# Kernel tuning notes

Hardware: AMD Instinct MI355X
Metric: run time of the kernel (lower is better)

Reference implementation:

```python
import math
import jax, jax.numpy as jnp
import numpy as np

EMBED_DIM = 1024
NUM_HEADS = 16
FACTOR = 5


def setup_inputs() -> dict:
    key = jax.random.key(0)
    kx, kw, kb, kow, kob = jax.random.split(key, 5)
    B, S, E = 8, 4096, EMBED_DIM
    scale = 1.0 / math.sqrt(E)
    x = jax.random.normal(kx, (B, S, E), dtype=jnp.float32)
    # nn.MultiheadAttention params: packed in_proj (q,k,v) and out_proj
    in_proj_w = jax.random.uniform(kw, (3 * E, E), dtype=jnp.float32, minval=-scale, maxval=scale)
    in_proj_b = jnp.zeros((3 * E,), dtype=jnp.float32)
    out_w = jax.random.uniform(kow, (E, E), dtype=jnp.float32, minval=-scale, maxval=scale)
    out_b = jnp.zeros((E,), dtype=jnp.float32)
    return {"x": x, "in_proj_w": in_proj_w, "in_proj_b": in_proj_b, "out_w": out_w, "out_b": out_b}


def reference(x, in_proj_w, in_proj_b, out_w, out_b):
    B, S, E = x.shape
    H = NUM_HEADS
    hd = E // H
    k = max(1, int(FACTOR * math.log(S + 1)))
    k = min(k, S)

    # top-k queries by L2 norm of each token
    energy = jnp.linalg.norm(x, axis=-1)            # [B, S]
    _, topk_idx = jax.lax.top_k(energy, k)          # [B, k]

    q_tok = jnp.take_along_axis(x, topk_idx[..., None], axis=1)  # [B, k, E]

    Wq, Wk, Wv = jnp.split(in_proj_w, 3, axis=0)    # each [E, E]
    bq, bk, bv = jnp.split(in_proj_b, 3, axis=0)

    q = (q_tok @ Wq.T + bq).reshape(B, k, H, hd)    # [B, k, H, hd]
    kk = (x @ Wk.T + bk).reshape(B, S, H, hd)       # [B, S, H, hd]
    v = (x @ Wv.T + bv).reshape(B, S, H, hd)

    scores = jnp.einsum("bqhd,bshd->bhqs", q, kk) / math.sqrt(hd)
    attn = jax.nn.softmax(scores, axis=-1)          # [B, H, k, S]
    ctx = jnp.einsum("bhqs,bshd->bqhd", attn, v).reshape(B, k, E)
    out_sel = ctx @ out_w.T + out_b                 # [B, k, E]

    # default value for non-selected positions: per-batch mean of x
    default = jnp.mean(x, axis=1)                   # [B, E]
    result = jnp.broadcast_to(default[:, None, :], (B, S, E))
    batch_ar = jnp.arange(B)[:, None]
    result = result.at[batch_ar, topk_idx].set(out_sel)
    return result
```

## Files before the change

kernel.cpp:

```cpp
#include <hip/hip_runtime.h>

using u16 = unsigned short;
using u32 = unsigned int;
using u64 = unsigned long long;
typedef __attribute__((ext_vector_type(8))) short s16x8;
typedef __attribute__((ext_vector_type(4))) short s16x4;
typedef __attribute__((ext_vector_type(4))) float f32x4;

__device__ __forceinline__ float bf2f(u16 u){ return __uint_as_float(((u32)u)<<16); }
__device__ __forceinline__ u16 f2bf(float f){
  u32 u = __float_as_uint(f);
  u += 0x7fffu + ((u>>16)&1u);
  return (u16)(u>>16);
}
__device__ __forceinline__ void gl_lds16(const void* g, void* l){
  __builtin_amdgcn_global_load_lds((const __attribute__((address_space(1))) void*)g,
                                   (__attribute__((address_space(3))) void*)l, 16, 0, 0);
}

__global__ __launch_bounds__(256) void k_cvt_all(const float* __restrict__ ipw, const float* __restrict__ ipb,
                                                 const float* __restrict__ outw,
                                                 u16* __restrict__ ipwb, u16* __restrict__ ipbb,
                                                 u16* __restrict__ outwb){
  int bid = blockIdx.x;
  const float* src; u16* dst; int n; int base;
  if (bid < 3072){ src=ipw; dst=ipwb; n=3145728; base=bid; }
  else if (bid < 3075){ src=ipb; dst=ipbb; n=3072; base=bid-3072; }
  else { src=outw; dst=outwb; n=1048576; base=bid-3075; }
  int i = (base*256 + threadIdx.x)*4;
  if (i >= n) return;
  float4 v = *(const float4*)(src + i);
  s16x4 o;
  o[0]=(short)f2bf(v.x); o[1]=(short)f2bf(v.y); o[2]=(short)f2bf(v.z); o[3]=(short)f2bf(v.w);
  *(s16x4*)(dst + i) = o;
}

__global__ __launch_bounds__(256) void k_prep_x(const float* __restrict__ x, u16* __restrict__ xb, float* __restrict__ energy){
  int tok = blockIdx.x*4 + (threadIdx.x>>6);
  int lane = threadIdx.x & 63;
  const float* p = x + (size_t)tok*1024 + lane*16;
  float4 a[4];
  #pragma unroll
  for (int j=0;j<4;++j) a[j] = ((const float4*)p)[j];
  float s = 0.f;
  s16x8 o0, o1;
  #pragma unroll
  for (int j=0;j<2;++j){
    o0[j*4+0]=(short)f2bf(a[j].x); o0[j*4+1]=(short)f2bf(a[j].y);
    o0[j*4+2]=(short)f2bf(a[j].z); o0[j*4+3]=(short)f2bf(a[j].w);
  }
  #pragma unroll
  for (int j=0;j<2;++j){
    o1[j*4+0]=(short)f2bf(a[2+j].x); o1[j*4+1]=(short)f2bf(a[2+j].y);
    o1[j*4+2]=(short)f2bf(a[2+j].z); o1[j*4+3]=(short)f2bf(a[2+j].w);
  }
  #pragma unroll
  for (int j=0;j<4;++j){
    s += a[j].x*a[j].x + a[j].y*a[j].y + a[j].z*a[j].z + a[j].w*a[j].w;
  }
  u16* xo = xb + (size_t)tok*1024 + lane*16;
  *(s16x8*)xo = o0;
  *(s16x8*)(xo+8) = o1;
  #pragma unroll
  for (int off=32; off; off>>=1) s += __shfl_xor(s, off);
  if (lane==0) energy[tok] = s;
}

__global__ __launch_bounds__(256) void k_colsum(const u16* __restrict__ xb, float* __restrict__ colsum){
  int b = blockIdx.x, sc = blockIdx.y;
  int t = threadIdx.x;
  float acc[4] = {0.f,0.f,0.f,0.f};
  for (int s = sc*128; s < sc*128+128; ++s){
    s16x4 v = *(const s16x4*)(xb + ((size_t)b*4096 + s)*1024 + t*4);
    #pragma unroll
    for (int i=0;i<4;++i) acc[i] += bf2f((u16)v[i]);
  }
  #pragma unroll
  for (int i=0;i<4;++i) atomicAdd(&colsum[b*1024 + t*4 + i], acc[i]);
}

__global__ __launch_bounds__(256) void k_topk(const float* __restrict__ energy, int* __restrict__ topk, int* __restrict__ sel){
  int b = blockIdx.x, t = threadIdx.x;
  int lane = t & 63, wid = t >> 6;
  __shared__ u64 wmax[4];
  __shared__ u64 winner;
  u64 v[16];
  #pragma unroll
  for (int i=0;i<16;++i){
    u32 tok = i*256 + t;
    float e = energy[b*4096 + tok];
    v[i] = ((u64)__float_as_uint(e) << 32) | (u32)(~tok);
    sel[b*4096 + tok] = -1;
  }
  __syncthreads();
  for (int it=0; it<41; ++it){
    u64 m = v[0];
    #pragma unroll
    for (int i=1;i<16;++i) m = v[i] > m ? v[i] : m;
    #pragma unroll
    for (int off=32; off; off>>=1){
      u64 o = __shfl_xor(m, off);
      m = o > m ? o : m;
    }
    if (lane==0) wmax[wid] = m;
    __syncthreads();
    if (t==0){
      u64 g = wmax[0];
      #pragma unroll
      for (int w=1;w<4;++w) g = wmax[w] > g ? wmax[w] : g;
      winner = g;
      u32 tok = (~(u32)g) & 4095u;
      topk[b*64+it] = (int)tok;
      sel[b*4096 + tok] = it;
    }
    __syncthreads();
    u32 wtok = (~(u32)winner) & 4095u;
    #pragma unroll
    for (int i=0;i<16;++i){
      if ((u32)(i*256 + t) == wtok) v[i] = 0;
    }
  }
}

__global__ __launch_bounds__(256) void k_gather_q(const float* __restrict__ x, const int* __restrict__ topk,
                                                  u16* __restrict__ Aq){
  int b = blockIdx.x, qi = blockIdx.y, t = threadIdx.x;
  size_t dst = ((size_t)(b*48+qi))*1024 + t*4;
  if (qi >= 41){ s16x4 z = {0,0,0,0}; *(s16x4*)&Aq[dst] = z; return; }
  int tok = topk[b*64+qi];
  float4 v = *(const float4*)(x + ((size_t)b*4096 + tok)*1024 + t*4);
  s16x4 o;
  o[0]=(short)f2bf(v.x); o[1]=(short)f2bf(v.y); o[2]=(short)f2bf(v.z); o[3]=(short)f2bf(v.w);
  *(s16x4*)&Aq[dst] = o;
}

__global__ __launch_bounds__(256) void k_gemm(const u16* __restrict__ A, const u16* __restrict__ Bk,
                                              const u16* __restrict__ Bv,
                                              const u16* __restrict__ biask, const u16* __restrict__ biasv,
                                              u16* __restrict__ C, int nbn, int ncols, int half, float cscale){
  __shared__ u16 As[128*64];
  __shared__ u16 Bs[128*64];
  const int tid = threadIdx.x;
  const int bn = blockIdx.x % nbn;
  const int bm = blockIdx.x / nbn;
  const int m0 = bm*128, n0 = bn*128;
  const u16* Bbase  = (n0 < half) ? (Bk + (size_t)n0*1024) : (Bv + (size_t)(n0-half)*1024);
  const u16* biasp  = (n0 < half) ? (biask + n0) : (biasv + (n0-half));
  const int lane = tid & 63;
  const int wave = tid >> 6;
  const int wr = wave >> 1, wc = wave & 1;
  const int fr = lane & 15;
  const int fq = lane >> 4;
  f32x4 acc[4][4] = {};
  for (int k0 = 0; k0 < 1024; k0 += 64){
    __syncthreads();
    #pragma unroll
    for (int j=0;j<4;++j){
      int idx = j*256 + tid;
      int r = idx>>3; int cc = (idx&7)*8;
      gl_lds16(A + (size_t)(m0+r)*1024 + k0 + cc, &As[r*64+cc]);
    }
    #pragma unroll
    for (int j=0;j<4;++j){
      int idx = j*256 + tid;
      int r = idx>>3; int cc = (idx&7)*8;
      gl_lds16(Bbase + (size_t)r*1024 + k0 + cc, &Bs[r*64+cc]);
    }
    __syncthreads();
    #pragma unroll
    for (int kk=0; kk<64; kk+=32){
      s16x8 af[4], bfv[4];
      #pragma unroll
      for (int m=0;m<4;++m) af[m] = *(const s16x8*)&As[(wr*64 + m*16 + fr)*64 + kk + fq*8];
      #pragma unroll
      for (int n=0;n<4;++n) bfv[n] = *(const s16x8*)&Bs[(wc*64 + n*16 + fr)*64 + kk + fq*8];
      #pragma unroll
      for (int m=0;m<4;++m)
        #pragma unroll
        for (int n=0;n<4;++n)
          acc[m][n] = __builtin_amdgcn_mfma_f32_16x16x32_bf16(af[m], bfv[n], acc[m][n], 0,0,0);
    }
  }
  #pragma unroll
  for (int n=0;n<4;++n){
    int cl = wc*64 + n*16 + fr;
    int col = n0 + cl;
    float bvv = bf2f(biasp[cl]);
    #pragma unroll
    for (int m=0;m<4;++m){
      int rowb = m0 + wr*64 + m*16 + fq*4;
      f32x4 v = acc[m][n];
      #pragma unroll
      for (int i=0;i<4;++i)
        C[(size_t)(rowb+i)*ncols + col] = f2bf((v[i]+bvv)*cscale);
    }
  }
}

__global__ __launch_bounds__(256) void k_gemm_sk(const u16* __restrict__ A, const u16* __restrict__ B,
                                                 float* __restrict__ Cacc){
  __shared__ u16 As[128*64];
  __shared__ u16 Bs[128*64];
  const int tid = threadIdx.x;
  const int bn = blockIdx.x & 7;
  const int bm = blockIdx.x >> 3;
  const int kc = blockIdx.y;
  const int m0 = bm*128, n0 = bn*128;
  const u16* Bbase = B + (size_t)n0*1024;
  const int lane = tid & 63;
  const int wave = tid >> 6;
  const int wr = wave >> 1, wc = wave & 1;
  const int fr = lane & 15;
  const int fq = lane >> 4;
  f32x4 acc[4][4] = {};
  for (int k0 = kc*256; k0 < kc*256+256; k0 += 64){
    __syncthreads();
    #pragma unroll
    for (int j=0;j<4;++j){
      int idx = j*256 + tid;
      int r = idx>>3; int cc = (idx&7)*8;
      gl_lds16(A + (size_t)(m0+r)*1024 + k0 + cc, &As[r*64+cc]);
    }
    #pragma unroll
    for (int j=0;j<4;++j){
      int idx = j*256 + tid;
      int r = idx>>3; int cc = (idx&7)*8;
      gl_lds16(Bbase + (size_t)r*1024 + k0 + cc, &Bs[r*64+cc]);
    }
    __syncthreads();
    #pragma unroll
    for (int kk=0; kk<64; kk+=32){
      s16x8 af[4], bfv[4];
      #pragma unroll
      for (int m=0;m<4;++m) af[m] = *(const s16x8*)&As[(wr*64 + m*16 + fr)*64 + kk + fq*8];
      #pragma unroll
      for (int n=0;n<4;++n) bfv[n] = *(const s16x8*)&Bs[(wc*64 + n*16 + fr)*64 + kk + fq*8];
      #pragma unroll
      for (int m=0;m<4;++m)
        #pragma unroll
        for (int n=0;n<4;++n)
          acc[m][n] = __builtin_amdgcn_mfma_f32_16x16x32_bf16(af[m], bfv[n], acc[m][n], 0,0,0);
    }
  }
  #pragma unroll
  for (int n=0;n<4;++n){
    int col = n0 + wc*64 + n*16 + fr;
    #pragma unroll
    for (int m=0;m<4;++m){
      int rowb = m0 + wr*64 + m*16 + fq*4;
      f32x4 v = acc[m][n];
      #pragma unroll
      for (int i=0;i<4;++i)
        atomicAdd(&Cacc[(size_t)(rowb+i)*1024 + col], v[i]);
    }
  }
}

__global__ __launch_bounds__(256) void k_qfinish(const float* __restrict__ qacc, const float* __restrict__ ipb,
                                                 u16* __restrict__ qbf){
  int i = (blockIdx.x*256 + threadIdx.x)*4;
  float4 a = *(const float4*)(qacc + i);
  int col = i & 1023;
  float4 bq = *(const float4*)(ipb + col);
  s16x4 o;
  o[0]=(short)f2bf((a.x+bq.x)*0.125f);
  o[1]=(short)f2bf((a.y+bq.y)*0.125f);
  o[2]=(short)f2bf((a.z+bq.z)*0.125f);
  o[3]=(short)f2bf((a.w+bq.w)*0.125f);
  *(s16x4*)(qbf + i) = o;
}

__device__ __forceinline__ void stageA4(const u16* __restrict__ A, int m0, int k0, u16* slot, int tid){
  #pragma unroll
  for (int j=0;j<2;++j){
    int idx = j*512 + tid;
    int row = idx>>2;
    int sc = (idx&3) ^ ((row>>1)&3);
    gl_lds16(A + (size_t)(m0+row)*1024 + k0 + sc*8, slot + (size_t)idx*8);
  }
}
__device__ __forceinline__ void stageB4(const u16* __restrict__ B, int k0, u16* slot, int tid){
  #pragma unroll
  for (int j=0;j<2;++j){
    int idx = j*512 + tid;
    int row = idx>>2;
    int sc = (idx&3) ^ ((row>>1)&3);
    gl_lds16(B + (size_t)row*1024 + k0 + sc*8, slot + 8192 + (size_t)idx*8);
  }
}
__device__ __forceinline__ s16x8 fragA4(const u16* slot, int row, int fq){
  int pc = fq ^ ((row>>1)&3);
  return *(const s16x8*)(slot + row*32 + pc*8);
}
__device__ __forceinline__ s16x8 fragB4(const u16* slot, int row, int fq){
  int pc = fq ^ ((row>>1)&3);
  return *(const s16x8*)(slot + 8192 + row*32 + pc*8);
}

#define KSTEP4(T, CA, CB, NA, NB)                                              \
  if ((T) < 29){                                                               \
    u16* ns = lds + (((T)+3)&3)*16384;                                         \
    stageA4(A, m0, ((T)+3)*32, ns, tid);                                       \
    stageB4(Bbase, ((T)+3)*32, ns, tid);                                       \
  }                                                                            \
  if ((T) < 29)      { asm volatile("s_waitcnt vmcnt(8)" ::: "memory"); }      \
  else if ((T)==29)  { asm volatile("s_waitcnt vmcnt(4)" ::: "memory"); }      \
  else if ((T)==30)  { asm volatile("s_waitcnt vmcnt(0)" ::: "memory"); }      \
  asm volatile("s_waitcnt lgkmcnt(0)" ::: "memory");                           \
  __builtin_amdgcn_sched_barrier(0);                                           \
  __builtin_amdgcn_s_barrier();                                                \
  __builtin_amdgcn_sched_barrier(0);                                           \
  if ((T) < 31){                                                               \
    const u16* rs = lds + (((T)+1)&3)*16384;                                   \
    _Pragma("unroll")                                                          \
    for (int m=0;m<8;++m) NA[m] = fragA4(rs, wm*128 + m*16 + fr, fq);          \
    _Pragma("unroll")                                                          \
    for (int n=0;n<4;++n) NB[n] = fragB4(rs, wn*64 + n*16 + fr, fq);           \
  }                                                                            \
  __builtin_amdgcn_sched_barrier(0);                                           \
  __builtin_amdgcn_s_setprio(1);                                               \
  _Pragma("unroll")                                                            \
  for (int m=0;m<8;++m)                                                        \
    _Pragma("unroll")                                                          \
    for (int n=0;n<4;++n)                                                      \
      acc[m][n] = __builtin_amdgcn_mfma_f32_16x16x32_bf16(CA[m], CB[n], acc[m][n], 0,0,0); \
  __builtin_amdgcn_s_setprio(0);

__global__ __launch_bounds__(512) void k_kvgemm4(const u16* __restrict__ A, const u16* __restrict__ Bk,
                                                 const u16* __restrict__ Bv,
                                                 const u16* __restrict__ biask, const u16* __restrict__ biasv,
                                                 u16* __restrict__ C){
  __shared__ u16 lds[4*16384];
  const int tid = threadIdx.x;
  const int sbid = ((int)blockIdx.x & 7)*128 + ((int)blockIdx.x >> 3);
  const int bn = sbid & 7;
  const int bm = sbid >> 3;
  const int m0 = bm*256, n0 = bn*256;
  const u16* Bbase = (bn < 4) ? (Bk + (size_t)n0*1024) : (Bv + (size_t)(n0-1024)*1024);
  const u16* biasp = (bn < 4) ? (biask + n0) : (biasv + (n0-1024));
  const int lane = tid & 63, wid = tid >> 6;
  const int wm = wid >> 2, wn = wid & 3;
  const int fr = lane & 15, fq = lane >> 4;
  f32x4 acc[8][4] = {};
  s16x8 afr0[8], bfr0[4], afr1[8], bfr1[4];

  stageA4(A, m0, 0, lds, tid);            stageB4(Bbase, 0, lds, tid);
  stageA4(A, m0, 32, lds+16384, tid);     stageB4(Bbase, 32, lds+16384, tid);
  stageA4(A, m0, 64, lds+2*16384, tid);   stageB4(Bbase, 64, lds+2*16384, tid);
  asm volatile("s_waitcnt vmcnt(8)" ::: "memory");
  __builtin_amdgcn_sched_barrier(0);
  __builtin_amdgcn_s_barrier();
  __builtin_amdgcn_sched_barrier(0);
  #pragma unroll
  for (int m=0;m<8;++m) afr0[m] = fragA4(lds, wm*128 + m*16 + fr, fq);
  #pragma unroll
  for (int n=0;n<4;++n) bfr0[n] = fragB4(lds, wn*64 + n*16 + fr, fq);

  for (int t=0; t<32; t+=2){
    KSTEP4(t,   afr0, bfr0, afr1, bfr1);
    KSTEP4(t+1, afr1, bfr1, afr0, bfr0);
  }

  u16* eLDS = lds;
  #pragma unroll
  for (int h=0; h<2; ++h){
    __syncthreads();
    if (wm == h){
      #pragma unroll
      for (int n=0;n<4;++n){
        int cl = wn*64 + n*16 + fr;
        float bvv = bf2f(biasp[cl]);
        #pragma unroll
        for (int m=0;m<8;++m){
          #pragma unroll
          for (int i=0;i<4;++i){
            int r = m*16 + fq*4 + i;
            eLDS[r*256 + cl] = f2bf(acc[m][n][i] + bvv);
          }
        }
      }
    }
    __syncthreads();
    #pragma unroll
    for (int j=0;j<8;++j){
      int e = j*512 + tid;
      int row = e >> 5, ch = e & 31;
      *(s16x8*)(C + (size_t)(m0 + h*128 + row)*2048 + n0 + ch*8) = *(const s16x8*)&eLDS[row*256 + ch*8];
    }
  }
}

__global__ __launch_bounds__(64) void k_attn(const u16* __restrict__ qb, const u16* __restrict__ KV,
                                             float* __restrict__ part_ctx, float* __restrict__ part_ml,
                                             int G, int hg0, int ncols, int half, int nt, int NSP){
  const int b = blockIdx.x / G, hl = blockIdx.x % G;
  const int h = hg0 + hl;
  const int bh = b*16 + h;
  const int sp = blockIdx.y;
  const int lane = threadIdx.x;
  const int fr = lane & 15, fq = lane >> 4;
  __shared__ u16 k_lds[64*72];
  __shared__ u16 v_lds[64*72];
  __shared__ u16 p_lds[48*72];
  s16x8 af[3][2];
  #pragma unroll
  for (int m=0;m<3;++m)
    #pragma unroll
    for (int kk=0;kk<2;++kk)
      af[m][kk] = *(const s16x8*)(qb + ((size_t)(b*48 + m*16 + fr))*1024 + h*64 + kk*32 + fq*8);
  f32x4 acc_o[3][4] = {};
  float m_run[3][4], l_run[3][4];
  #pragma unroll
  for (int m=0;m<3;++m)
    #pragma unroll
    for (int i=0;i<4;++i){ m_run[m][i] = -3e38f; l_run[m][i] = 0.f; }

  for (int it=0; it<nt; ++it){
    int s0 = (sp*nt + it)*64;
    __syncthreads();
    #pragma unroll
    for (int j=0;j<8;++j){
      int r = j*8 + (lane>>3);
      int sg = (lane&7)*8;
      const u16* kp = KV + ((size_t)(b*4096 + s0 + r))*ncols + hl*64 + sg;
      *(s16x8*)&k_lds[r*72+sg] = *(const s16x8*)kp;
      *(s16x8*)&v_lds[r*72+sg] = *(const s16x8*)(kp+half);
    }
    __syncthreads();
    f32x4 sc4[3][4] = {};
    #pragma unroll
    for (int kk=0;kk<2;++kk){
      s16x8 bk[4];
      #pragma unroll
      for (int n=0;n<4;++n)
        bk[n] = *(const s16x8*)&k_lds[(n*16+fr)*72 + kk*32 + fq*8];
      #pragma unroll
      for (int m=0;m<3;++m)
        #pragma unroll
        for (int n=0;n<4;++n)
          sc4[m][n] = __builtin_amdgcn_mfma_f32_16x16x32_bf16(af[m][kk], bk[n], sc4[m][n], 0,0,0);
    }
    #pragma unroll
    for (int m=0;m<3;++m){
      #pragma unroll
      for (int i=0;i<4;++i){
        float rmax = fmaxf(fmaxf(sc4[m][0][i], sc4[m][1][i]), fmaxf(sc4[m][2][i], sc4[m][3][i]));
        #pragma unroll
        for (int off=1; off<16; off<<=1) rmax = fmaxf(rmax, __shfl_xor(rmax, off));
        float mnew = fmaxf(m_run[m][i], rmax);
        float alpha = __expf(m_run[m][i] - mnew);
        m_run[m][i] = mnew;
        float rsum = 0.f;
        #pragma unroll
        for (int n=0;n<4;++n){
          float p = __expf(sc4[m][n][i] - mnew);
          rsum += p;
          p_lds[(m*16 + fq*4 + i)*72 + n*16 + fr] = f2bf(p);
        }
        #pragma unroll
        for (int off=1; off<16; off<<=1) rsum += __shfl_xor(rsum, off);
        l_run[m][i] = l_run[m][i]*alpha + rsum;
        #pragma unroll
        for (int n=0;n<4;++n) acc_o[m][n][i] *= alpha;
      }
    }
    __syncthreads();
    #pragma unroll
    for (int kk=0;kk<2;++kk){
      s16x8 ap[3];
      #pragma unroll
      for (int m=0;m<3;++m)
        ap[m] = *(const s16x8*)&p_lds[(m*16+fr)*72 + kk*32 + fq*8];
      #pragma unroll
      for (int n=0;n<4;++n){
        s16x8 bv;
        #pragma unroll
        for (int i2=0;i2<8;++i2)
          bv[i2] = (short)v_lds[(kk*32 + fq*8 + i2)*72 + n*16 + fr];
        #pragma unroll
        for (int m=0;m<3;++m)
          acc_o[m][n] = __builtin_amdgcn_mfma_f32_16x16x32_bf16(ap[m], bv, acc_o[m][n], 0,0,0);
      }
    }
  }
  size_t pbase = ((size_t)(bh*NSP + sp))*48*64;
  #pragma unroll
  for (int m=0;m<3;++m)
    #pragma unroll
    for (int n=0;n<4;++n)
      #pragma unroll
      for (int i=0;i<4;++i){
        int qi = m*16 + fq*4 + i, d = n*16 + fr;
        part_ctx[pbase + (size_t)qi*64 + d] = acc_o[m][n][i];
      }
  if (fr==0){
    #pragma unroll
    for (int m=0;m<3;++m)
      #pragma unroll
      for (int i=0;i<4;++i){
        int qi = m*16 + fq*4 + i;
        part_ml[((size_t)(bh*NSP+sp))*96 + qi*2+0] = m_run[m][i];
        part_ml[((size_t)(bh*NSP+sp))*96 + qi*2+1] = l_run[m][i];
      }
  }
}

__global__ __launch_bounds__(64) void k_combine(const float* __restrict__ part_ctx, const float* __restrict__ part_ml,
                                                u16* __restrict__ ctxb, int NSP){
  int bh = blockIdx.x, qi = blockIdx.y;
  int b = bh>>4, h = bh&15;
  int lane = threadIdx.x;
  size_t dst = ((size_t)(b*48+qi))*1024 + h*64 + lane;
  if (qi >= 41){ ctxb[dst] = 0; return; }
  float M = -3e38f;
  for (int p=0;p<NSP;++p)
    M = fmaxf(M, part_ml[((size_t)(bh*NSP+p))*96 + qi*2+0]);
  float l = 0.f, c = 0.f;
  for (int p=0;p<NSP;++p){
    float pm = part_ml[((size_t)(bh*NSP+p))*96 + qi*2+0];
    float pl = part_ml[((size_t)(bh*NSP+p))*96 + qi*2+1];
    float w = __expf(pm-M);
    l += pl*w;
    c += w * part_ctx[((size_t)(bh*NSP+p))*48*64 + (size_t)qi*64 + lane];
  }
  ctxb[dst] = f2bf(c / l);
}

__global__ __launch_bounds__(256) void k_finalize(const float* __restrict__ oacc, const float* __restrict__ outb,
                                                  const float* __restrict__ colsum,
                                                  const int* __restrict__ sel, float* __restrict__ out){
  int row = blockIdx.x;
  int b = row >> 12;
  int t = threadIdx.x;
  int s = sel[row];
  float4 o;
  if (s >= 0){
    float4 a = *(const float4*)(oacc + ((size_t)(b*48+s))*1024 + t*4);
    float4 bb = *(const float4*)(outb + t*4);
    o.x = a.x+bb.x; o.y = a.y+bb.y; o.z = a.z+bb.z; o.w = a.w+bb.w;
  } else {
    o = *(const float4*)(colsum + b*1024 + t*4);
    o.x *= (1.f/4096.f); o.y *= (1.f/4096.f); o.z *= (1.f/4096.f); o.w *= (1.f/4096.f);
  }
  *(float4*)(out + (size_t)row*1024 + t*4) = o;
}

extern "C" void kernel_launch(void* const* d_in, const int* in_sizes, int n_in,
                              void* d_out, int out_size, void* d_ws, size_t ws_size,
                              hipStream_t stream) {
  const float* x    = (const float*)d_in[0];
  const float* ipw  = (const float*)d_in[1];
  const float* ipb  = (const float*)d_in[2];
  const float* outw = (const float*)d_in[3];
  const float* outb = (const float*)d_in[4];
  float* out = (float*)d_out;
  char* ws = (char*)d_ws;

  const int cfgG[7]   = {16, 8, 4, 2, 1, 1, 1};
  const int cfgNSP[7] = {16,16,16,16,16, 4, 2};
  int G = 1, NSP = 2;
  size_t oXB=0,oWIP=0,oBIP=0,oWO=0,oEN=0,oCS=0,oTK=0,oSEL=0,oAQ=0,oQB=0,oCTXB=0,oQA=0,oOA=0,oPML=0,oPCTX=0,oKV=0;
  for (int ci=0; ci<7; ++ci){
    int g = cfgG[ci], nsp = cfgNSP[ci];
    size_t o = 0;
    size_t xb=o;   o += 67108864;
    size_t wip=o;  o += 6291456;
    size_t bip=o;  o += 6144;
    size_t wo=o;   o += 2097152;
    size_t en=o;   o += 131072;
    size_t cs=o;   o += 32768;
    size_t tk=o;   o += 2048;
    size_t sl=o;   o += 131072;
    size_t aq=o;   o += 786432;
    size_t qb=o;   o += 786432;
    size_t cb=o;   o += 786432;
    size_t qa=o;   o += 1572864;
    size_t oa=o;   o += 1572864;
    size_t pm=o;   o += (size_t)nsp*49152;
    size_t pc=o;   o += (size_t)nsp*1572864;
    size_t kv=o;   o += (size_t)g*8388608;
    if (o <= ws_size || ci == 6){
      G=g; NSP=nsp;
      oXB=xb; oWIP=wip; oBIP=bip; oWO=wo; oEN=en; oCS=cs; oTK=tk; oSEL=sl;
      oAQ=aq; oQB=qb; oCTXB=cb; oQA=qa; oOA=oa; oPML=pm; oPCTX=pc; oKV=kv;
      break;
    }
  }

  u16*   xb     = (u16*)(ws + oXB);
  u16*   ipwb   = (u16*)(ws + oWIP);
  u16*   ipbb   = (u16*)(ws + oBIP);
  u16*   outwb  = (u16*)(ws + oWO);
  float* energy = (float*)(ws + oEN);
  float* colsum = (float*)(ws + oCS);
  int*   topk   = (int*)(ws + oTK);
  int*   sel    = (int*)(ws + oSEL);
  u16*   Aq     = (u16*)(ws + oAQ);
  u16*   qbf    = (u16*)(ws + oQB);
  u16*   ctxb   = (u16*)(ws + oCTXB);
  float* qacc   = (float*)(ws + oQA);
  float* oacc   = (float*)(ws + oOA);
  float* pml    = (float*)(ws + oPML);
  float* pctx   = (float*)(ws + oPCTX);
  u16*   KV     = (u16*)(ws + oKV);

  hipMemsetAsync(colsum, 0, 32768, stream);
  hipMemsetAsync(qacc, 0, 1572864, stream);
  hipMemsetAsync(oacc, 0, 1572864, stream);

  k_cvt_all <<<4099, 256, 0, stream>>>(ipw, ipb, outw, ipwb, ipbb, outwb);

  k_prep_x <<<8192, 256, 0, stream>>>(x, xb, energy);
  k_colsum <<<dim3(8,32), 256, 0, stream>>>(xb, colsum);
  k_topk   <<<8, 256, 0, stream>>>(energy, topk, sel);
  k_gather_q<<<dim3(8,48), 256, 0, stream>>>(x, topk, Aq);

  k_gemm_sk <<<dim3(24,4), 256, 0, stream>>>(Aq, ipwb, qacc);
  k_qfinish <<<384, 256, 0, stream>>>(qacc, ipb, qbf);

  if (G == 16){
    const int nt = 64/NSP;
    k_kvgemm4 <<<1024, 512, 0, stream>>>(xb,
        ipwb + (size_t)1024*1024, ipwb + (size_t)2048*1024,
        ipbb + 1024, ipbb + 2048, KV);
    k_attn <<<dim3(128, NSP), 64, 0, stream>>>(qbf, KV, pctx, pml, 16, 0, 2048, 1024, nt, NSP);
  } else {
    const int nchunk = 16 / G;
    const int ncols = G*128, half = G*64, nt = 64/NSP;
    for (int c=0; c<nchunk; ++c){
      int hg0 = c*G;
      k_gemm <<<G*256, 256, 0, stream>>>(
          xb,
          ipwb + (size_t)(1024 + hg0*64)*1024,
          ipwb + (size_t)(2048 + hg0*64)*1024,
          ipbb + 1024 + hg0*64,
          ipbb + 2048 + hg0*64,
          KV, G, ncols, half, 1.0f);
      k_attn <<<dim3(8*G, NSP), 64, 0, stream>>>(qbf, KV, pctx, pml, G, hg0, ncols, half, nt, NSP);
    }
  }

  k_combine<<<dim3(128,48), 64, 0, stream>>>(pctx, pml, ctxb, NSP);

  k_gemm_sk <<<dim3(24,4), 256, 0, stream>>>(ctxb, outwb, oacc);

  k_finalize<<<32768, 256, 0, stream>>>(oacc, outb, colsum, sel, out);
}
```

Before: 385.3 us.

## Restructure KV GEMM into double-buffered BK=64 pipeline with interleaved staging

Replaces the 4-slot BK=32 KV projection GEMM with a 2-slot BK=64 variant. Each k-step now loads fragments in halves, interleaves MFMA groups with barriers, and issues the next tile's global-to-LDS loads between compute phases, using a row-XOR swizzle over 8 chunks. The goal is fewer barriers per unit of K and better overlap of loads with MFMA. It also merges three memsets into one by making the zeroed buffers contiguous. The extra barriers inside each step, and a shallower prefetch depth, could expose memory latency.

```diff
diff --git a/kernel.cpp b/kernel.cpp
--- a/kernel.cpp
+++ b/kernel.cpp
@@ -17,6 +17,8 @@
   __builtin_amdgcn_global_load_lds((const __attribute__((address_space(1))) void*)g,
                                    (__attribute__((address_space(3))) void*)l, 16, 0, 0);
 }
+#define SCHED0 __builtin_amdgcn_sched_barrier(0)
+#define BAR    __builtin_amdgcn_s_barrier()
 
 __global__ __launch_bounds__(256) void k_cvt_all(const float* __restrict__ ipw, const float* __restrict__ ipb,
                                                  const float* __restrict__ outw,
@@ -270,95 +272,109 @@
   *(s16x4*)(qbf + i) = o;
 }
 
-__device__ __forceinline__ void stageA4(const u16* __restrict__ A, int m0, int k0, u16* slot, int tid){
-  #pragma unroll
-  for (int j=0;j<2;++j){
+__device__ __forceinline__ void stage5(const u16* __restrict__ src, int k0, u16* dst, int tid){
+  #pragma unroll
+  for (int j=0;j<4;++j){
     int idx = j*512 + tid;
-    int row = idx>>2;
-    int sc = (idx&3) ^ ((row>>1)&3);
-    gl_lds16(A + (size_t)(m0+row)*1024 + k0 + sc*8, slot + (size_t)idx*8);
-  }
-}
-__device__ __forceinline__ void stageB4(const u16* __restrict__ B, int k0, u16* slot, int tid){
-  #pragma unroll
-  for (int j=0;j<2;++j){
-    int idx = j*512 + tid;
-    int row = idx>>2;
-    int sc = (idx&3) ^ ((row>>1)&3);
-    gl_lds16(B + (size_t)row*1024 + k0 + sc*8, slot + 8192 + (size_t)idx*8);
-  }
-}
-__device__ __forceinline__ s16x8 fragA4(const u16* slot, int row, int fq){
-  int pc = fq ^ ((row>>1)&3);
-  return *(const s16x8*)(slot + row*32 + pc*8);
-}
-__device__ __forceinline__ s16x8 fragB4(const u16* slot, int row, int fq){
-  int pc = fq ^ ((row>>1)&3);
-  return *(const s16x8*)(slot + 8192 + row*32 + pc*8);
-}
-
-#define KSTEP4(T, CA, CB, NA, NB)                                              \
-  if ((T) < 29){                                                               \
-    u16* ns = lds + (((T)+3)&3)*16384;                                         \
-    stageA4(A, m0, ((T)+3)*32, ns, tid);                                       \
-    stageB4(Bbase, ((T)+3)*32, ns, tid);                                       \
-  }                                                                            \
-  if ((T) < 29)      { asm volatile("s_waitcnt vmcnt(8)" ::: "memory"); }      \
-  else if ((T)==29)  { asm volatile("s_waitcnt vmcnt(4)" ::: "memory"); }      \
-  else if ((T)==30)  { asm volatile("s_waitcnt vmcnt(0)" ::: "memory"); }      \
-  asm volatile("s_waitcnt lgkmcnt(0)" ::: "memory");                           \
-  __builtin_amdgcn_sched_barrier(0);                                           \
-  __builtin_amdgcn_s_barrier();                                                \
-  __builtin_amdgcn_sched_barrier(0);                                           \
-  if ((T) < 31){                                                               \
-    const u16* rs = lds + (((T)+1)&3)*16384;                                   \
-    _Pragma("unroll")                                                          \
-    for (int m=0;m<8;++m) NA[m] = fragA4(rs, wm*128 + m*16 + fr, fq);          \
-    _Pragma("unroll")                                                          \
-    for (int n=0;n<4;++n) NB[n] = fragB4(rs, wn*64 + n*16 + fr, fq);           \
-  }                                                                            \
-  __builtin_amdgcn_sched_barrier(0);                                           \
-  __builtin_amdgcn_s_setprio(1);                                               \
-  _Pragma("unroll")                                                            \
-  for (int m=0;m<8;++m)                                                        \
-    _Pragma("unroll")                                                          \
-    for (int n=0;n<4;++n)                                                      \
-      acc[m][n] = __builtin_amdgcn_mfma_f32_16x16x32_bf16(CA[m], CB[n], acc[m][n], 0,0,0); \
-  __builtin_amdgcn_s_setprio(0);
-
-__global__ __launch_bounds__(512) void k_kvgemm4(const u16* __restrict__ A, const u16* __restrict__ Bk,
+    int row = idx>>3, ch = idx&7;
+    gl_lds16(src + (size_t)row*1024 + k0 + ((ch^(row&7))<<3), dst + (size_t)idx*8);
+  }
+}
+__device__ __forceinline__ s16x8 frag5(const u16* base, int row, int kh, int fq){
+  int ch = (kh*4+fq) ^ (row&7);
+  return *(const s16x8*)(base + row*64 + ch*8);
+}
+
+__global__ __launch_bounds__(512) void k_kvgemm5(const u16* __restrict__ A, const u16* __restrict__ Bk,
                                                  const u16* __restrict__ Bv,
                                                  const u16* __restrict__ biask, const u16* __restrict__ biasv,
                                                  u16* __restrict__ C){
-  __shared__ u16 lds[4*16384];
+  __shared__ u16 lds[65536];
   const int tid = threadIdx.x;
   const int sbid = ((int)blockIdx.x & 7)*128 + ((int)blockIdx.x >> 3);
   const int bn = sbid & 7;
   const int bm = sbid >> 3;
   const int m0 = bm*256, n0 = bn*256;
+  const u16* Asrc  = A + (size_t)m0*1024;
   const u16* Bbase = (bn < 4) ? (Bk + (size_t)n0*1024) : (Bv + (size_t)(n0-1024)*1024);
   const u16* biasp = (bn < 4) ? (biask + n0) : (biasv + (n0-1024));
   const int lane = tid & 63, wid = tid >> 6;
   const int wm = wid >> 2, wn = wid & 3;
   const int fr = lane & 15, fq = lane >> 4;
   f32x4 acc[8][4] = {};
-  s16x8 afr0[8], bfr0[4], afr1[8], bfr1[4];
-
-  stageA4(A, m0, 0, lds, tid);            stageB4(Bbase, 0, lds, tid);
-  stageA4(A, m0, 32, lds+16384, tid);     stageB4(Bbase, 32, lds+16384, tid);
-  stageA4(A, m0, 64, lds+2*16384, tid);   stageB4(Bbase, 64, lds+2*16384, tid);
+
+  stage5(Asrc, 0, lds, tid);          stage5(Bbase, 0, lds+16384, tid);
+  stage5(Asrc, 64, lds+32768, tid);   stage5(Bbase, 64, lds+49152, tid);
   asm volatile("s_waitcnt vmcnt(8)" ::: "memory");
-  __builtin_amdgcn_sched_barrier(0);
-  __builtin_amdgcn_s_barrier();
-  __builtin_amdgcn_sched_barrier(0);
-  #pragma unroll
-  for (int m=0;m<8;++m) afr0[m] = fragA4(lds, wm*128 + m*16 + fr, fq);
-  #pragma unroll
-  for (int n=0;n<4;++n) bfr0[n] = fragB4(lds, wn*64 + n*16 + fr, fq);
-
-  for (int t=0; t<32; t+=2){
-    KSTEP4(t,   afr0, bfr0, afr1, bfr1);
-    KSTEP4(t+1, afr1, bfr1, afr0, bfr0);
+  SCHED0; BAR; SCHED0;
+
+  for (int t=0; t<16; ++t){
+    const u16* bA = lds + (t&1)*32768;
+    const u16* bB = bA + 16384;
+    u16* nA = (u16*)bA;
+    u16* nB = (u16*)bB;
+    s16x8 a[8][2], b[4][2];
+    #pragma unroll
+    for (int m=0;m<4;++m){
+      a[m][0] = frag5(bA, wm*128 + m*16 + fr, 0, fq);
+      a[m][1] = frag5(bA, wm*128 + m*16 + fr, 1, fq);
+    }
+    #pragma unroll
+    for (int n=0;n<4;++n) b[n][0] = frag5(bB, wn*64 + n*16 + fr, 0, fq);
+    SCHED0; BAR; SCHED0;
+    asm volatile("s_waitcnt lgkmcnt(0)" ::: "memory");
+    SCHED0;
+    __builtin_amdgcn_s_setprio(1);
+    #pragma unroll
+    for (int m=0;m<4;++m)
+      #pragma unroll
+      for (int n=0;n<4;++n)
+        acc[m][n] = __builtin_amdgcn_mfma_f32_16x16x32_bf16(a[m][0], b[n][0], acc[m][n], 0,0,0);
+    __builtin_amdgcn_s_setprio(0);
+    SCHED0; BAR; SCHED0;
+    #pragma unroll
+    for (int m=4;m<8;++m){
+      a[m][0] = frag5(bA, wm*128 + m*16 + fr, 0, fq);
+      a[m][1] = frag5(bA, wm*128 + m*16 + fr, 1, fq);
+    }
+    #pragma unroll
+    for (int n=0;n<4;++n) b[n][1] = frag5(bB, wn*64 + n*16 + fr, 1, fq);
+    SCHED0; BAR; SCHED0;
+    asm volatile("s_waitcnt lgkmcnt(0)" ::: "memory");
+    SCHED0;
+    __builtin_amdgcn_s_setprio(1);
+    #pragma unroll
+    for (int m=0;m<4;++m)
+      #pragma unroll
+      for (int n=0;n<4;++n)
+        acc[m][n] = __builtin_amdgcn_mfma_f32_16x16x32_bf16(a[m][1], b[n][1], acc[m][n], 0,0,0);
+    __builtin_amdgcn_s_setprio(0);
+    SCHED0; BAR; SCHED0;
+    if (t < 14) stage5(Asrc, (t+2)*64, nA, tid);
+    SCHED0; BAR; SCHED0;
+    __builtin_amdgcn_s_setprio(1);
+    #pragma unroll
+    for (int m=4;m<8;++m)
+      #pragma unroll
+      for (int n=0;n<4;++n)
+        acc[m][n] = __builtin_amdgcn_mfma_f32_16x16x32_bf16(a[m][0], b[n][0], acc[m][n], 0,0,0);
+    __builtin_amdgcn_s_setprio(0);
+    SCHED0; BAR; SCHED0;
+    if (t < 14) stage5(Bbase, (t+2)*64, nB, tid);
+    SCHED0;
+    __builtin_amdgcn_s_setprio(1);
+    #pragma unroll
+    for (int m=4;m<8;++m)
+      #pragma unroll
+      for (int n=0;n<4;++n)
+        acc[m][n] = __builtin_amdgcn_mfma_f32_16x16x32_bf16(a[m][1], b[n][1], acc[m][n], 0,0,0);
+    __builtin_amdgcn_s_setprio(0);
+    if (t < 14){
+      asm volatile("s_waitcnt vmcnt(8)" ::: "memory");
+    } else if (t == 14){
+      asm volatile("s_waitcnt vmcnt(0)" ::: "memory");
+    }
+    SCHED0; BAR; SCHED0;
   }
 
   u16* eLDS = lds;
@@ -559,7 +575,7 @@
   const int cfgG[7]   = {16, 8, 4, 2, 1, 1, 1};
   const int cfgNSP[7] = {16,16,16,16,16, 4, 2};
   int G = 1, NSP = 2;
-  size_t oXB=0,oWIP=0,oBIP=0,oWO=0,oEN=0,oCS=0,oTK=0,oSEL=0,oAQ=0,oQB=0,oCTXB=0,oQA=0,oOA=0,oPML=0,oPCTX=0,oKV=0;
+  size_t oXB=0,oWIP=0,oBIP=0,oWO=0,oEN=0,oCS=0,oQA=0,oOA=0,oTK=0,oSEL=0,oAQ=0,oQB=0,oCTXB=0,oPML=0,oPCTX=0,oKV=0;
   for (int ci=0; ci<7; ++ci){
     int g = cfgG[ci], nsp = cfgNSP[ci];
     size_t o = 0;
@@ -569,20 +585,20 @@
     size_t wo=o;   o += 2097152;
     size_t en=o;   o += 131072;
     size_t cs=o;   o += 32768;
+    size_t qa=o;   o += 1572864;
+    size_t oa=o;   o += 1572864;
     size_t tk=o;   o += 2048;
     size_t sl=o;   o += 131072;
     size_t aq=o;   o += 786432;
     size_t qb=o;   o += 786432;
     size_t cb=o;   o += 786432;
-    size_t qa=o;   o += 1572864;
-    size_t oa=o;   o += 1572864;
     size_t pm=o;   o += (size_t)nsp*49152;
     size_t pc=o;   o += (size_t)nsp*1572864;
     size_t kv=o;   o += (size_t)g*8388608;
     if (o <= ws_size || ci == 6){
       G=g; NSP=nsp;
-      oXB=xb; oWIP=wip; oBIP=bip; oWO=wo; oEN=en; oCS=cs; oTK=tk; oSEL=sl;
-      oAQ=aq; oQB=qb; oCTXB=cb; oQA=qa; oOA=oa; oPML=pm; oPCTX=pc; oKV=kv;
+      oXB=xb; oWIP=wip; oBIP=bip; oWO=wo; oEN=en; oCS=cs; oQA=qa; oOA=oa; oTK=tk; oSEL=sl;
+      oAQ=aq; oQB=qb; oCTXB=cb; oPML=pm; oPCTX=pc; oKV=kv;
       break;
     }
   }
@@ -593,20 +609,18 @@
   u16*   outwb  = (u16*)(ws + oWO);
   float* energy = (float*)(ws + oEN);
   float* colsum = (float*)(ws + oCS);
+  float* qacc   = (float*)(ws + oQA);
+  float* oacc   = (float*)(ws + oOA);
   int*   topk   = (int*)(ws + oTK);
   int*   sel    = (int*)(ws + oSEL);
   u16*   Aq     = (u16*)(ws + oAQ);
   u16*   qbf    = (u16*)(ws + oQB);
   u16*   ctxb   = (u16*)(ws + oCTXB);
-  float* qacc   = (float*)(ws + oQA);
-  float* oacc   = (float*)(ws + oOA);
   float* pml    = (float*)(ws + oPML);
   float* pctx   = (float*)(ws + oPCTX);
   u16*   KV     = (u16*)(ws + oKV);
 
-  hipMemsetAsync(colsum, 0, 32768, stream);
-  hipMemsetAsync(qacc, 0, 1572864, stream);
-  hipMemsetAsync(oacc, 0, 1572864, stream);
+  hipMemsetAsync(colsum, 0, 32768 + 2*1572864, stream);
 
   k_cvt_all <<<4099, 256, 0, stream>>>(ipw, ipb, outw, ipwb, ipbb, outwb);
 
@@ -620,7 +634,7 @@
 
   if (G == 16){
     const int nt = 64/NSP;
-    k_kvgemm4 <<<1024, 512, 0, stream>>>(xb,
+    k_kvgemm5 <<<1024, 512, 0, stream>>>(xb,
         ipwb + (size_t)1024*1024, ipwb + (size_t)2048*1024,
         ipbb + 1024, ipbb + 2048, KV);
     k_attn <<<dim3(128, NSP), 64, 0, stream>>>(qbf, KV, pctx, pml, 16, 0, 2048, 1024, nt, NSP);
```

New measurement: 387.4 us. Within noise of the previous version (+0.5%).
